# Kernel tuning notes

Hardware: AMD Instinct MI355X
Metric: run time of the kernel (lower is better)

Reference implementation:

```python
import jax, jax.numpy as jnp
import numpy as np

N_HEADS = 16
ROPE_THETA = 10000.0


def setup_inputs() -> dict:
    key = jax.random.key(0)
    k1, k2, k3 = jax.random.split(key, 3)
    B, T, C = 1, 4096, 1024
    d_k = C // N_HEADS
    x = jax.random.normal(k1, (B, T, C), dtype=jnp.float32)
    # RoPE frequencies: freqs_cis = exp(i * t * theta^{-2j/d_k}), stored as cos/sin
    inv_freq = 1.0 / (ROPE_THETA ** (jnp.arange(0, d_k, 2, dtype=jnp.float32) / d_k))  # (d_k//2,)
    t = jnp.arange(T, dtype=jnp.float32)
    angles = jnp.outer(t, inv_freq)  # (T, d_k//2)
    freqs_cos = jnp.cos(angles)
    freqs_sin = jnp.sin(angles)
    W_attn = jax.random.normal(k2, (C, 3 * C), dtype=jnp.float32) * 0.02  # x @ W_attn == Linear(C,3C,bias=False)
    W_proj = jax.random.normal(k3, (C, C), dtype=jnp.float32) * 0.02
    return {"x": x, "freqs_cos": freqs_cos, "freqs_sin": freqs_sin, "W_attn": W_attn, "W_proj": W_proj}


def _rope(x, cos, sin):
    # x: (B, H, T, d_k); cos/sin: (T, d_k//2). Interleaved-pair rotation
    # matching torch.view_as_complex on (..., d_k//2, 2).
    xr = x.reshape(*x.shape[:-1], -1, 2)
    x0, x1 = xr[..., 0], xr[..., 1]
    c = cos[None, None, :, :]
    s = sin[None, None, :, :]
    o0 = x0 * c - x1 * s
    o1 = x0 * s + x1 * c
    return jnp.stack([o0, o1], axis=-1).reshape(x.shape)


def reference(x, freqs_cos, freqs_sin, W_attn, W_proj):
    B, T, C = x.shape
    H = N_HEADS
    d_k = C // H
    qkv = x @ W_attn  # (B, T, 3C)
    q, k, v = jnp.split(qkv, 3, axis=-1)
    q = q.reshape(B, T, H, d_k).transpose(0, 2, 1, 3)  # (B, H, T, d_k)
    k = k.reshape(B, T, H, d_k).transpose(0, 2, 1, 3)
    v = v.reshape(B, T, H, d_k).transpose(0, 2, 1, 3)
    q = _rope(q, freqs_cos[:T], freqs_sin[:T])
    k = _rope(k, freqs_cos[:T], freqs_sin[:T])
    scale = 1.0 / jnp.sqrt(jnp.asarray(d_k, dtype=x.dtype))
    att = jnp.einsum("bhqd,bhkd->bhqk", q, k) * scale  # (B, H, T, T)
    causal = jnp.tril(jnp.ones((T, T), dtype=bool))
    att = jnp.where(causal[None, None, :, :], att, -jnp.inf)
    att = jax.nn.softmax(att, axis=-1)
    y = jnp.einsum("bhqk,bhkd->bhqd", att, v)  # (B, H, T, d_k)
    y = y.transpose(0, 2, 1, 3).reshape(B, T, C)
    return y @ W_proj
```

## Files before the change

kernel.cpp:

```cpp
#include <hip/hip_runtime.h>

using f32x4  = __attribute__((ext_vector_type(4))) float;
using bf16x4 = __attribute__((ext_vector_type(4))) __bf16;
using bf16x8 = __attribute__((ext_vector_type(8))) __bf16;
using s16x4  = __attribute__((ext_vector_type(4))) short;

__device__ inline void gload16(const void* g, void* l) {
  __builtin_amdgcn_global_load_lds((const __attribute__((address_space(1))) void*)g,
                                   (__attribute__((address_space(3))) void*)l, 16, 0, 0);
}

__device__ inline f32x4 mfma16x16x16bf(bf16x4 a, bf16x4 b, f32x4 c) {
#if __has_builtin(__builtin_amdgcn_mfma_f32_16x16x16_bf16)
  return __builtin_amdgcn_mfma_f32_16x16x16_bf16(a, b, c, 0, 0, 0);
#else
  return __builtin_amdgcn_mfma_f32_16x16x16bf16_1k(__builtin_bit_cast(s16x4, a),
                                                   __builtin_bit_cast(s16x4, b), c, 0, 0, 0);
#endif
}

__global__ __launch_bounds__(256) void pack_bf16_kernel(const float* __restrict__ in,
                                                        __bf16* __restrict__ out, int n4) {
  int i = blockIdx.x * 256 + threadIdx.x;
  if (i >= n4) return;
  f32x4 v = ((const f32x4*)in)[i];
  bf16x4 o;
  o[0] = (__bf16)v[0]; o[1] = (__bf16)v[1]; o[2] = (__bf16)v[2]; o[3] = (__bf16)v[3];
  ((bf16x4*)out)[i] = o;
}

__global__ __launch_bounds__(256) void transpose_bf16_kernel(const float* __restrict__ in,
                                                             __bf16* __restrict__ out,
                                                             int R, int C) {
  __shared__ float tile[32][33];
  int c0 = blockIdx.x * 32, r0 = blockIdx.y * 32;
  int tx = threadIdx.x, ty = threadIdx.y;
  #pragma unroll
  for (int i = 0; i < 32; i += 8)
    tile[ty + i][tx] = in[(size_t)(r0 + ty + i) * C + c0 + tx];
  __syncthreads();
  #pragma unroll
  for (int i = 0; i < 32; i += 8)
    out[(size_t)(c0 + ty + i) * R + r0 + tx] = (__bf16)tile[tx][ty + i];
}

template <typename OUT>
__global__ __launch_bounds__(256) void gemm_bt_kernel(const __bf16* __restrict__ A,
                                                      const __bf16* __restrict__ Bt,
                                                      OUT* __restrict__ C,
                                                      int M, int N, int K) {
  const int bn = blockIdx.x * 128, bm = blockIdx.y * 128;
  const int tid = threadIdx.x;
  const int lane = tid & 63, wid = tid >> 6;
  const int wm = (wid >> 1) * 64, wn = (wid & 1) * 64;
  const int l15 = lane & 15, lhi = lane >> 4;
  __shared__ __align__(16) __bf16 As[2][4096];
  __shared__ __align__(16) __bf16 Bs[2][4096];
  f32x4 acc[4][4] = {};

  const int rrow = wid * 16 + (lane >> 2);
  const int schunk = lane & 3;

  #define G_STAGE(k0_, b_)                                                              \
    {                                                                                   \
      _Pragma("unroll")                                                                 \
      for (int i_ = 0; i_ < 2; ++i_) {                                                  \
        int row_ = i_ * 64 + rrow;                                                      \
        int lch_ = schunk ^ (row_ & 3);                                                 \
        gload16(A + (size_t)(bm + row_) * K + (k0_) + lch_ * 8,                         \
                (char*)&As[b_][0] + i_ * 4096 + wid * 1024);                            \
        gload16(Bt + (size_t)(bn + row_) * K + (k0_) + lch_ * 8,                        \
                (char*)&Bs[b_][0] + i_ * 4096 + wid * 1024);                            \
      }                                                                                 \
    }

  G_STAGE(0, 0);
  __syncthreads();
  const int nk = K >> 5;
  for (int t = 0; t < nk; ++t) {
    const int cur = t & 1;
    if (t + 1 < nk) G_STAGE((t + 1) * 32, cur ^ 1);
    bf16x8 af[4], bfr[4];
    #pragma unroll
    for (int i = 0; i < 4; ++i) {
      int row = wm + i * 16 + l15;
      af[i] = *(const bf16x8*)&As[cur][row * 32 + ((lhi ^ (row & 3)) * 8)];
    }
    #pragma unroll
    for (int j = 0; j < 4; ++j) {
      int row = wn + j * 16 + l15;
      bfr[j] = *(const bf16x8*)&Bs[cur][row * 32 + ((lhi ^ (row & 3)) * 8)];
    }
    #pragma unroll
    for (int i = 0; i < 4; ++i)
      #pragma unroll
      for (int j = 0; j < 4; ++j)
        acc[i][j] = __builtin_amdgcn_mfma_f32_16x16x32_bf16(af[i], bfr[j], acc[i][j], 0, 0, 0);
    __syncthreads();
  }
  #pragma unroll
  for (int i = 0; i < 4; ++i)
    #pragma unroll
    for (int j = 0; j < 4; ++j)
      #pragma unroll
      for (int r = 0; r < 4; ++r)
        C[(size_t)(bm + wm + i * 16 + lhi * 4 + r) * N + (bn + wn + j * 16 + l15)] =
            (OUT)acc[i][j][r];
  #undef G_STAGE
}

__global__ __launch_bounds__(256) void postproc_kernel(const __bf16* __restrict__ qkv,
                                                       const float* __restrict__ fc,
                                                       const float* __restrict__ fs,
                                                       __bf16* __restrict__ qb,
                                                       __bf16* __restrict__ kst,
                                                       __bf16* __restrict__ vst) {
  const int ktile = blockIdx.x, h = blockIdx.y;
  const int tid = threadIdx.x;
  const int row = tid >> 2, seg = tid & 3;
  const int t = ktile * 64 + row;
  __shared__ __bf16 vt[64][72];

  float cs[8], sn[8];
  #pragma unroll
  for (int p = 0; p < 8; ++p) {
    cs[p] = fc[t * 32 + seg * 8 + p];
    sn[p] = fs[t * 32 + seg * 8 + p];
  }
  const float QS = 0.125f * 1.4426950408889634f;

  {
    const __bf16* src = qkv + (size_t)t * 3072 + h * 64 + seg * 16;
    bf16x8 a = *(const bf16x8*)src, b = *(const bf16x8*)(src + 8);
    float v[16];
    #pragma unroll
    for (int i = 0; i < 8; ++i) { v[i] = (float)a[i]; v[8 + i] = (float)b[i]; }
    __bf16 ob[16];
    #pragma unroll
    for (int p = 0; p < 8; ++p) {
      ob[2 * p]     = (__bf16)((v[2 * p] * cs[p] - v[2 * p + 1] * sn[p]) * QS);
      ob[2 * p + 1] = (__bf16)((v[2 * p] * sn[p] + v[2 * p + 1] * cs[p]) * QS);
    }
    __bf16* dst = qb + (size_t)t * 1024 + h * 64 + seg * 16;
    *(bf16x8*)dst = *(bf16x8*)ob;
    *(bf16x8*)(dst + 8) = *(bf16x8*)(ob + 8);
  }
  {
    const __bf16* src = qkv + (size_t)t * 3072 + 1024 + h * 64 + seg * 16;
    bf16x8 a = *(const bf16x8*)src, b = *(const bf16x8*)(src + 8);
    float v[16];
    #pragma unroll
    for (int i = 0; i < 8; ++i) { v[i] = (float)a[i]; v[8 + i] = (float)b[i]; }
    __bf16 ob[16];
    #pragma unroll
    for (int p = 0; p < 8; ++p) {
      ob[2 * p]     = (__bf16)(v[2 * p] * cs[p] - v[2 * p + 1] * sn[p]);
      ob[2 * p + 1] = (__bf16)(v[2 * p] * sn[p] + v[2 * p + 1] * cs[p]);
    }
    __bf16* kdst = kst + ((size_t)(h * 64 + ktile)) * 4096 + row * 64;
    const int r7 = row & 7;
    *(bf16x8*)(kdst + ((seg * 2) ^ r7) * 8)     = *(bf16x8*)ob;
    *(bf16x8*)(kdst + ((seg * 2 + 1) ^ r7) * 8) = *(bf16x8*)(ob + 8);
  }
  {
    const __bf16* src = qkv + (size_t)t * 3072 + 2048 + h * 64 + seg * 16;
    *(bf16x8*)&vt[row][seg * 16]     = *(const bf16x8*)src;
    *(bf16x8*)&vt[row][seg * 16 + 8] = *(const bf16x8*)(src + 8);
  }
  __syncthreads();
  {
    const int d = tid >> 2, q4 = tid & 3;
    __bf16 tb[16];
    #pragma unroll
    for (int j = 0; j < 16; ++j) tb[j] = vt[q4 * 16 + j][d];
    __bf16* vdst = vst + ((size_t)(h * 64 + ktile)) * 4096 + d * 64;
    const int r7 = d & 7;
    *(bf16x8*)(vdst + ((q4 * 2) ^ r7) * 8)     = *(bf16x8*)tb;
    *(bf16x8*)(vdst + ((q4 * 2 + 1) ^ r7) * 8) = *(bf16x8*)(tb + 8);
  }
}

__global__ __launch_bounds__(256) void fattn_kernel(const __bf16* __restrict__ qb,
                                                    const __bf16* __restrict__ kst,
                                                    const __bf16* __restrict__ vst,
                                                    __bf16* __restrict__ yb) {
  const int b = blockIdx.x;
  const int xcd = b & 7, slot = b >> 3;
  const int head = xcd * 2 + (slot & 1);
  const int qt = 63 - (slot >> 1);
  const int tid = threadIdx.x, lane = tid & 63, w = tid >> 6;
  const int c16 = lane & 15, g = lane >> 4;

  __shared__ __align__(16) __bf16 kls[2][4096];
  __shared__ __align__(16) __bf16 vls[2][4096];

  const __bf16* ktiles = kst + (size_t)head * 64 * 4096;
  const __bf16* vtiles = vst + (size_t)head * 64 * 4096;

  #define F_STAGE(kt_, b_)                                                        \
    {                                                                             \
      const char* kb_ = (const char*)(ktiles + (size_t)(kt_) * 4096);             \
      const char* vb_ = (const char*)(vtiles + (size_t)(kt_) * 4096);             \
      _Pragma("unroll")                                                           \
      for (int i_ = 0; i_ < 2; ++i_) {                                            \
        int off_ = i_ * 4096 + w * 1024;                                          \
        gload16(kb_ + off_ + lane * 16, (char*)&kls[b_][0] + off_);               \
        gload16(vb_ + off_ + lane * 16, (char*)&vls[b_][0] + off_);               \
      }                                                                           \
    }

  const int qw0 = qt * 64 + w * 16;

  bf16x8 qf[2];
  #pragma unroll
  for (int kc = 0; kc < 2; ++kc)
    qf[kc] = *(const bf16x8*)(qb + (size_t)(qw0 + c16) * 1024 + head * 64 + kc * 32 + g * 8);

  f32x4 o[4] = {};
  f32x4 ol = {};
  bf16x4 ones1;
  ones1[0] = ones1[1] = ones1[2] = ones1[3] = (__bf16)1.0f;

  F_STAGE(0, 0);
  __syncthreads();

  for (int kt = 0; kt <= qt; ++kt) {
    const int cur = kt & 1;
    if (kt < qt) F_STAGE(kt + 1, cur ^ 1);
    f32x4 s[4];
    __builtin_amdgcn_s_setprio(1);
    #pragma unroll
    for (int st = 0; st < 4; ++st) {
      const __bf16* kr = &kls[cur][(st * 16 + c16) * 64];
      bf16x8 ka0 = *(const bf16x8*)&kr[((g) ^ (c16 & 7)) * 8];
      bf16x8 ka1 = *(const bf16x8*)&kr[((4 + g) ^ (c16 & 7)) * 8];
      f32x4 z = {};
      z = __builtin_amdgcn_mfma_f32_16x16x32_bf16(ka0, qf[0], z, 0, 0, 0);
      s[st] = __builtin_amdgcn_mfma_f32_16x16x32_bf16(ka1, qf[1], z, 0, 0, 0);
    }
    __builtin_amdgcn_s_setprio(0);
    if (kt == qt) {
      const int qloc = w * 16 + c16;
      #pragma unroll
      for (int st = 0; st < 4; ++st)
        #pragma unroll
        for (int r = 0; r < 4; ++r)
          if (st * 16 + g * 4 + r > qloc) s[st][r] = -1e30f;
    }
    bf16x4 pb[4];
    #pragma unroll
    for (int st = 0; st < 4; ++st) {
      bf16x4 pv;
      #pragma unroll
      for (int r = 0; r < 4; ++r) pv[r] = (__bf16)exp2f(s[st][r]);
      pb[st] = pv;
    }
    __builtin_amdgcn_s_setprio(1);
    #pragma unroll
    for (int st = 0; st < 4; ++st) {
      ol = mfma16x16x16bf(ones1, pb[st], ol);
      #pragma unroll
      for (int dt = 0; dt < 4; ++dt) {
        const int vrow = dt * 16 + c16;
        const int loff = vrow * 64 + (((2 * st + (g >> 1)) ^ (c16 & 7)) * 8) + (g & 1) * 4;
        bf16x4 va = *(const bf16x4*)&vls[cur][loff];
        o[dt] = mfma16x16x16bf(va, pb[st], o[dt]);
      }
    }
    __builtin_amdgcn_s_setprio(0);
    __syncthreads();
  }
  const float inv = 1.f / ol[0];
  const int q = qw0 + c16;
  #pragma unroll
  for (int dt = 0; dt < 4; ++dt) {
    bf16x4 ov;
    #pragma unroll
    for (int r = 0; r < 4; ++r) ov[r] = (__bf16)(o[dt][r] * inv);
    *(bf16x4*)(yb + (size_t)q * 1024 + head * 64 + dt * 16 + g * 4) = ov;
  }
  #undef F_STAGE
}

extern "C" void kernel_launch(void* const* d_in, const int* in_sizes, int n_in,
                              void* d_out, int out_size, void* d_ws, size_t ws_size,
                              hipStream_t stream) {
  const float* x  = (const float*)d_in[0];
  const float* fc = (const float*)d_in[1];
  const float* fs = (const float*)d_in[2];
  const float* Wa = (const float*)d_in[3];
  const float* Wp = (const float*)d_in[4];
  float* out = (float*)d_out;

  char* ws = (char*)d_ws;
  __bf16* x_bf   = (__bf16*)(ws);
  __bf16* Wa_t   = (__bf16*)(ws + 8388608);
  __bf16* Wp_t   = (__bf16*)(ws + 14680064);
  __bf16* y_bf   = (__bf16*)(ws + 16777216);
  __bf16* qkv_bf = (__bf16*)(ws + 25165824);
  __bf16* kst    = (__bf16*)(ws + 50331648);
  __bf16* vst    = (__bf16*)(ws + 58720256);
  __bf16* q_bf   = x_bf;

  pack_bf16_kernel<<<4096, 256, 0, stream>>>(x, x_bf, 1048576);
  transpose_bf16_kernel<<<dim3(96, 32), dim3(32, 8), 0, stream>>>(Wa, Wa_t, 1024, 3072);
  transpose_bf16_kernel<<<dim3(32, 32), dim3(32, 8), 0, stream>>>(Wp, Wp_t, 1024, 1024);
  gemm_bt_kernel<__bf16><<<dim3(24, 32), 256, 0, stream>>>(x_bf, Wa_t, qkv_bf, 4096, 3072, 1024);
  postproc_kernel<<<dim3(64, 16), 256, 0, stream>>>(qkv_bf, fc, fs, q_bf, kst, vst);
  fattn_kernel<<<1024, 256, 0, stream>>>(q_bf, kst, vst, y_bf);
  gemm_bt_kernel<float><<<dim3(8, 32), 256, 0, stream>>>(y_bf, Wp_t, out, 4096, 1024, 1024);
}
```

Before: 230.4 us.

## Enlarge attention query tile to 128 rows and remap GEMM blocks across XCDs

The flash-attention kernel now uses 512-thread blocks, each covering 128 query rows, so every K/V tile staged in LDS is shared by eight waves instead of four. This halves the global K/V traffic per query. Waves whose causal limit ends one tile early skip compute on the final tile. The GEMM kernels switch to a 1D grid with an XCD-aware block remapping so that neighbouring tiles land on the same XCD for better L2 reuse. The trade-offs are fewer, larger attention blocks, which can hurt load balance and occupancy, and idle waves on the last tile.

```diff
diff --git a/kernel.cpp b/kernel.cpp
--- a/kernel.cpp
+++ b/kernel.cpp
@@ -49,7 +49,12 @@
                                                       const __bf16* __restrict__ Bt,
                                                       OUT* __restrict__ C,
                                                       int M, int N, int K) {
-  const int bn = blockIdx.x * 128, bm = blockIdx.y * 128;
+  const int nwg = gridDim.x, flat = blockIdx.x;
+  const int cpx = nwg >> 3;
+  const int wg = (flat & 7) * cpx + (flat >> 3);
+  const int nbn = N >> 7;
+  const int bn = (wg % nbn) * 128, bm = (wg / nbn) * 128;
+
   const int tid = threadIdx.x;
   const int lane = tid & 63, wid = tid >> 6;
   const int wm = (wid >> 1) * 64, wn = (wid & 1) * 64;
@@ -180,14 +185,14 @@
   }
 }
 
-__global__ __launch_bounds__(256) void fattn_kernel(const __bf16* __restrict__ qb,
+__global__ __launch_bounds__(512) void fattn_kernel(const __bf16* __restrict__ qb,
                                                     const __bf16* __restrict__ kst,
                                                     const __bf16* __restrict__ vst,
                                                     __bf16* __restrict__ yb) {
   const int b = blockIdx.x;
   const int xcd = b & 7, slot = b >> 3;
   const int head = xcd * 2 + (slot & 1);
-  const int qt = 63 - (slot >> 1);
+  const int qt = 31 - (slot >> 1);
   const int tid = threadIdx.x, lane = tid & 63, w = tid >> 6;
   const int c16 = lane & 15, g = lane >> 4;
 
@@ -201,15 +206,14 @@
     {                                                                             \
       const char* kb_ = (const char*)(ktiles + (size_t)(kt_) * 4096);             \
       const char* vb_ = (const char*)(vtiles + (size_t)(kt_) * 4096);             \
-      _Pragma("unroll")                                                           \
-      for (int i_ = 0; i_ < 2; ++i_) {                                            \
-        int off_ = i_ * 4096 + w * 1024;                                          \
-        gload16(kb_ + off_ + lane * 16, (char*)&kls[b_][0] + off_);               \
-        gload16(vb_ + off_ + lane * 16, (char*)&vls[b_][0] + off_);               \
-      }                                                                           \
-    }
-
-  const int qw0 = qt * 64 + w * 16;
+      gload16(kb_ + w * 1024 + lane * 16, (char*)&kls[b_][0] + w * 1024);         \
+      gload16(vb_ + w * 1024 + lane * 16, (char*)&vls[b_][0] + w * 1024);         \
+    }
+
+  const int qw0 = qt * 128 + w * 16;
+  const int lastkt = 2 * qt + 1;
+  const int wlast = 2 * qt + (w >> 2);
+  const int maskbase = w * 16 + c16 - (w >> 2) * 64;
 
   bf16x8 qf[2];
   #pragma unroll
@@ -224,50 +228,51 @@
   F_STAGE(0, 0);
   __syncthreads();
 
-  for (int kt = 0; kt <= qt; ++kt) {
+  for (int kt = 0; kt <= lastkt; ++kt) {
     const int cur = kt & 1;
-    if (kt < qt) F_STAGE(kt + 1, cur ^ 1);
-    f32x4 s[4];
-    __builtin_amdgcn_s_setprio(1);
-    #pragma unroll
-    for (int st = 0; st < 4; ++st) {
-      const __bf16* kr = &kls[cur][(st * 16 + c16) * 64];
-      bf16x8 ka0 = *(const bf16x8*)&kr[((g) ^ (c16 & 7)) * 8];
-      bf16x8 ka1 = *(const bf16x8*)&kr[((4 + g) ^ (c16 & 7)) * 8];
-      f32x4 z = {};
-      z = __builtin_amdgcn_mfma_f32_16x16x32_bf16(ka0, qf[0], z, 0, 0, 0);
-      s[st] = __builtin_amdgcn_mfma_f32_16x16x32_bf16(ka1, qf[1], z, 0, 0, 0);
-    }
-    __builtin_amdgcn_s_setprio(0);
-    if (kt == qt) {
-      const int qloc = w * 16 + c16;
-      #pragma unroll
-      for (int st = 0; st < 4; ++st)
+    if (kt < lastkt) F_STAGE(kt + 1, cur ^ 1);
+    if (kt <= wlast) {
+      f32x4 s[4];
+      __builtin_amdgcn_s_setprio(1);
+      #pragma unroll
+      for (int st = 0; st < 4; ++st) {
+        const __bf16* kr = &kls[cur][(st * 16 + c16) * 64];
+        bf16x8 ka0 = *(const bf16x8*)&kr[((g) ^ (c16 & 7)) * 8];
+        bf16x8 ka1 = *(const bf16x8*)&kr[((4 + g) ^ (c16 & 7)) * 8];
+        f32x4 z = {};
+        z = __builtin_amdgcn_mfma_f32_16x16x32_bf16(ka0, qf[0], z, 0, 0, 0);
+        s[st] = __builtin_amdgcn_mfma_f32_16x16x32_bf16(ka1, qf[1], z, 0, 0, 0);
+      }
+      __builtin_amdgcn_s_setprio(0);
+      if (kt == wlast) {
         #pragma unroll
-        for (int r = 0; r < 4; ++r)
-          if (st * 16 + g * 4 + r > qloc) s[st][r] = -1e30f;
-    }
-    bf16x4 pb[4];
-    #pragma unroll
-    for (int st = 0; st < 4; ++st) {
-      bf16x4 pv;
-      #pragma unroll
-      for (int r = 0; r < 4; ++r) pv[r] = (__bf16)exp2f(s[st][r]);
-      pb[st] = pv;
-    }
-    __builtin_amdgcn_s_setprio(1);
-    #pragma unroll
-    for (int st = 0; st < 4; ++st) {
-      ol = mfma16x16x16bf(ones1, pb[st], ol);
-      #pragma unroll
-      for (int dt = 0; dt < 4; ++dt) {
-        const int vrow = dt * 16 + c16;
-        const int loff = vrow * 64 + (((2 * st + (g >> 1)) ^ (c16 & 7)) * 8) + (g & 1) * 4;
-        bf16x4 va = *(const bf16x4*)&vls[cur][loff];
-        o[dt] = mfma16x16x16bf(va, pb[st], o[dt]);
+        for (int st = 0; st < 4; ++st)
+          #pragma unroll
+          for (int r = 0; r < 4; ++r)
+            if (st * 16 + g * 4 + r > maskbase) s[st][r] = -1e30f;
       }
-    }
-    __builtin_amdgcn_s_setprio(0);
+      bf16x4 pb[4];
+      #pragma unroll
+      for (int st = 0; st < 4; ++st) {
+        bf16x4 pv;
+        #pragma unroll
+        for (int r = 0; r < 4; ++r) pv[r] = (__bf16)exp2f(s[st][r]);
+        pb[st] = pv;
+      }
+      __builtin_amdgcn_s_setprio(1);
+      #pragma unroll
+      for (int st = 0; st < 4; ++st) {
+        ol = mfma16x16x16bf(ones1, pb[st], ol);
+        #pragma unroll
+        for (int dt = 0; dt < 4; ++dt) {
+          const int vrow = dt * 16 + c16;
+          const int loff = vrow * 64 + (((2 * st + (g >> 1)) ^ (c16 & 7)) * 8) + (g & 1) * 4;
+          bf16x4 va = *(const bf16x4*)&vls[cur][loff];
+          o[dt] = mfma16x16x16bf(va, pb[st], o[dt]);
+        }
+      }
+      __builtin_amdgcn_s_setprio(0);
+    }
     __syncthreads();
   }
   const float inv = 1.f / ol[0];
@@ -305,8 +310,8 @@
   pack_bf16_kernel<<<4096, 256, 0, stream>>>(x, x_bf, 1048576);
   transpose_bf16_kernel<<<dim3(96, 32), dim3(32, 8), 0, stream>>>(Wa, Wa_t, 1024, 3072);
   transpose_bf16_kernel<<<dim3(32, 32), dim3(32, 8), 0, stream>>>(Wp, Wp_t, 1024, 1024);
-  gemm_bt_kernel<__bf16><<<dim3(24, 32), 256, 0, stream>>>(x_bf, Wa_t, qkv_bf, 4096, 3072, 1024);
+  gemm_bt_kernel<__bf16><<<768, 256, 0, stream>>>(x_bf, Wa_t, qkv_bf, 4096, 3072, 1024);
   postproc_kernel<<<dim3(64, 16), 256, 0, stream>>>(qkv_bf, fc, fs, q_bf, kst, vst);
-  fattn_kernel<<<1024, 256, 0, stream>>>(q_bf, kst, vst, y_bf);
-  gemm_bt_kernel<float><<<dim3(8, 32), 256, 0, stream>>>(y_bf, Wp_t, out, 4096, 1024, 1024);
-}
+  fattn_kernel<<<512, 512, 0, stream>>>(q_bf, kst, vst, y_bf);
+  gemm_bt_kernel<float><<<256, 256, 0, stream>>>(y_bf, Wp_t, out, 4096, 1024, 1024);
+}
```

Measured after the change: 241.5 us. +4.8%, slower.

## Remap GEMM workgroups across XCDs and unroll attention loop by two buffers

Applied to the files above, without the earlier changes.

The GEMM kernel now takes a 1D grid and remaps the flat block index so that consecutive tiles land on the same XCD (stride-8 interleave), which is meant to improve L2 reuse of the A/B tiles. The flash-attention main loop is manually unrolled by two with compile-time buffer indices and precomputed LDS pointers. This removes the per-iteration swizzle arithmetic, and the exp2 step is interleaved per subtile with its PV MFMAs so exp work can overlap with matrix ops. The costs are larger code size and more register pressure, and the remap assumes the grid size is divisible by 8.

```diff
diff --git a/kernel.cpp b/kernel.cpp
--- a/kernel.cpp
+++ b/kernel.cpp
@@ -49,7 +49,12 @@
                                                       const __bf16* __restrict__ Bt,
                                                       OUT* __restrict__ C,
                                                       int M, int N, int K) {
-  const int bn = blockIdx.x * 128, bm = blockIdx.y * 128;
+  const int nwg = gridDim.x, flat = blockIdx.x;
+  const int cpx = nwg >> 3;
+  const int wg = (flat & 7) * cpx + (flat >> 3);
+  const int nbn = N >> 7;
+  const int bn = (wg % nbn) * 128, bm = (wg / nbn) * 128;
+
   const int tid = threadIdx.x;
   const int lane = tid & 63, wid = tid >> 6;
   const int wm = (wid >> 1) * 64, wn = (wid & 1) * 64;
@@ -221,55 +226,73 @@
   bf16x4 ones1;
   ones1[0] = ones1[1] = ones1[2] = ones1[3] = (__bf16)1.0f;
 
+  const int m7 = c16 & 7, h2 = g >> 1, lo4 = (g & 1) * 4;
+  const __bf16* kp0 = &kls[0][c16 * 64 + ((g ^ m7) * 8)];
+  const __bf16* kp1 = &kls[0][c16 * 64 + (((4 + g) ^ m7) * 8)];
+  const __bf16* vp0 = &vls[0][c16 * 64 + lo4 + (((0 + h2) ^ m7) * 8)];
+  const __bf16* vp1 = &vls[0][c16 * 64 + lo4 + (((2 + h2) ^ m7) * 8)];
+  const __bf16* vp2 = &vls[0][c16 * 64 + lo4 + (((4 + h2) ^ m7) * 8)];
+  const __bf16* vp3 = &vls[0][c16 * 64 + lo4 + (((6 + h2) ^ m7) * 8)];
+
+  #define F_ONE_ST(B_, st_, vp_)                                                  \
+    {                                                                             \
+      bf16x4 pv;                                                                  \
+      _Pragma("unroll")                                                           \
+      for (int r = 0; r < 4; ++r) pv[r] = (__bf16)exp2f(s[st_][r]);               \
+      __builtin_amdgcn_s_setprio(1);                                              \
+      ol = mfma16x16x16bf(ones1, pv, ol);                                         \
+      _Pragma("unroll")                                                           \
+      for (int dt = 0; dt < 4; ++dt) {                                            \
+        bf16x4 va = *(const bf16x4*)(vp_ + (B_) * 4096 + dt * 1024);              \
+        o[dt] = mfma16x16x16bf(va, pv, o[dt]);                                    \
+      }                                                                           \
+      __builtin_amdgcn_s_setprio(0);                                              \
+    }
+
+  #define F_COMPUTE(B_, kt_)                                                      \
+    {                                                                             \
+      f32x4 s[4];                                                                 \
+      __builtin_amdgcn_s_setprio(1);                                              \
+      _Pragma("unroll")                                                           \
+      for (int st = 0; st < 4; ++st) {                                            \
+        bf16x8 ka0 = *(const bf16x8*)(kp0 + (B_) * 4096 + st * 1024);             \
+        bf16x8 ka1 = *(const bf16x8*)(kp1 + (B_) * 4096 + st * 1024);             \
+        f32x4 z = {};                                                             \
+        z = __builtin_amdgcn_mfma_f32_16x16x32_bf16(ka0, qf[0], z, 0, 0, 0);      \
+        s[st] = __builtin_amdgcn_mfma_f32_16x16x32_bf16(ka1, qf[1], z, 0, 0, 0);  \
+      }                                                                           \
+      __builtin_amdgcn_s_setprio(0);                                              \
+      if ((kt_) == qt) {                                                          \
+        const int qloc = w * 16 + c16;                                            \
+        _Pragma("unroll")                                                         \
+        for (int st = 0; st < 4; ++st)                                            \
+          _Pragma("unroll")                                                       \
+          for (int r = 0; r < 4; ++r)                                             \
+            if (st * 16 + g * 4 + r > qloc) s[st][r] = -1e30f;                    \
+      }                                                                           \
+      F_ONE_ST(B_, 0, vp0)                                                        \
+      F_ONE_ST(B_, 1, vp1)                                                        \
+      F_ONE_ST(B_, 2, vp2)                                                        \
+      F_ONE_ST(B_, 3, vp3)                                                        \
+    }
+
   F_STAGE(0, 0);
   __syncthreads();
 
-  for (int kt = 0; kt <= qt; ++kt) {
-    const int cur = kt & 1;
-    if (kt < qt) F_STAGE(kt + 1, cur ^ 1);
-    f32x4 s[4];
-    __builtin_amdgcn_s_setprio(1);
-    #pragma unroll
-    for (int st = 0; st < 4; ++st) {
-      const __bf16* kr = &kls[cur][(st * 16 + c16) * 64];
-      bf16x8 ka0 = *(const bf16x8*)&kr[((g) ^ (c16 & 7)) * 8];
-      bf16x8 ka1 = *(const bf16x8*)&kr[((4 + g) ^ (c16 & 7)) * 8];
-      f32x4 z = {};
-      z = __builtin_amdgcn_mfma_f32_16x16x32_bf16(ka0, qf[0], z, 0, 0, 0);
-      s[st] = __builtin_amdgcn_mfma_f32_16x16x32_bf16(ka1, qf[1], z, 0, 0, 0);
-    }
-    __builtin_amdgcn_s_setprio(0);
-    if (kt == qt) {
-      const int qloc = w * 16 + c16;
-      #pragma unroll
-      for (int st = 0; st < 4; ++st)
-        #pragma unroll
-        for (int r = 0; r < 4; ++r)
-          if (st * 16 + g * 4 + r > qloc) s[st][r] = -1e30f;
-    }
-    bf16x4 pb[4];
-    #pragma unroll
-    for (int st = 0; st < 4; ++st) {
-      bf16x4 pv;
-      #pragma unroll
-      for (int r = 0; r < 4; ++r) pv[r] = (__bf16)exp2f(s[st][r]);
-      pb[st] = pv;
-    }
-    __builtin_amdgcn_s_setprio(1);
-    #pragma unroll
-    for (int st = 0; st < 4; ++st) {
-      ol = mfma16x16x16bf(ones1, pb[st], ol);
-      #pragma unroll
-      for (int dt = 0; dt < 4; ++dt) {
-        const int vrow = dt * 16 + c16;
-        const int loff = vrow * 64 + (((2 * st + (g >> 1)) ^ (c16 & 7)) * 8) + (g & 1) * 4;
-        bf16x4 va = *(const bf16x4*)&vls[cur][loff];
-        o[dt] = mfma16x16x16bf(va, pb[st], o[dt]);
-      }
-    }
-    __builtin_amdgcn_s_setprio(0);
+  int kt = 0;
+  while (true) {
+    if (kt < qt) F_STAGE(kt + 1, 1);
+    F_COMPUTE(0, kt)
     __syncthreads();
-  }
+    if (kt == qt) break;
+    ++kt;
+    if (kt < qt) F_STAGE(kt + 1, 0);
+    F_COMPUTE(1, kt)
+    __syncthreads();
+    if (kt == qt) break;
+    ++kt;
+  }
+
   const float inv = 1.f / ol[0];
   const int q = qw0 + c16;
   #pragma unroll
@@ -280,6 +303,8 @@
     *(bf16x4*)(yb + (size_t)q * 1024 + head * 64 + dt * 16 + g * 4) = ov;
   }
   #undef F_STAGE
+  #undef F_COMPUTE
+  #undef F_ONE_ST
 }
 
 extern "C" void kernel_launch(void* const* d_in, const int* in_sizes, int n_in,
@@ -305,8 +330,8 @@
   pack_bf16_kernel<<<4096, 256, 0, stream>>>(x, x_bf, 1048576);
   transpose_bf16_kernel<<<dim3(96, 32), dim3(32, 8), 0, stream>>>(Wa, Wa_t, 1024, 3072);
   transpose_bf16_kernel<<<dim3(32, 32), dim3(32, 8), 0, stream>>>(Wp, Wp_t, 1024, 1024);
-  gemm_bt_kernel<__bf16><<<dim3(24, 32), 256, 0, stream>>>(x_bf, Wa_t, qkv_bf, 4096, 3072, 1024);
+  gemm_bt_kernel<__bf16><<<768, 256, 0, stream>>>(x_bf, Wa_t, qkv_bf, 4096, 3072, 1024);
   postproc_kernel<<<dim3(64, 16), 256, 0, stream>>>(qkv_bf, fc, fs, q_bf, kst, vst);
   fattn_kernel<<<1024, 256, 0, stream>>>(q_bf, kst, vst, y_bf);
-  gemm_bt_kernel<float><<<dim3(8, 32), 256, 0, stream>>>(y_bf, Wp_t, out, 4096, 1024, 1024);
-}
+  gemm_bt_kernel<float><<<256, 256, 0, stream>>>(y_bf, Wp_t, out, 4096, 1024, 1024);
+}
```

Result: faster. 225.1 us (-2.3%).
